# Kernel optimization log

Hardware: AMD Instinct MI355X
Metric: run time of the kernel (lower is better)

## Reference

```python
import jax, jax.numpy as jnp
import numpy as np

DIM = 2048
N_HEADS = 32
N_KV_HEADS = 8
HEAD_DIM = DIM // N_HEADS
N_REP = N_HEADS // N_KV_HEADS
BSZ, SEQ = 2, 2048


def setup_inputs() -> dict:
    key = jax.random.key(0)
    ks = jax.random.split(key, 6)
    hidden_states = jax.random.normal(ks[0], (BSZ, SEQ, DIM), jnp.float32)
    # additive causal mask [1,1,S,S]
    causal = jnp.tril(jnp.ones((SEQ, SEQ), jnp.bool_))
    attention_mask = jnp.where(causal, 0.0, -1e9).astype(jnp.float32)[None, None]
    # RoPE tables [S, head_dim]
    inv_freq = 1.0 / (10000.0 ** (np.arange(0, HEAD_DIM, 2, dtype=np.float32) / HEAD_DIM))
    t = np.arange(SEQ, dtype=np.float32)
    freqs = np.outer(t, inv_freq)  # [S, head_dim/2]
    emb = np.concatenate([freqs, freqs], axis=-1)  # [S, head_dim]
    position_cos = jnp.asarray(np.cos(emb), jnp.float32)
    position_sin = jnp.asarray(np.sin(emb), jnp.float32)
    s = 0.02
    Wq = jax.random.normal(ks[1], (DIM, DIM), jnp.float32) * s
    Wk = jax.random.normal(ks[2], (N_KV_HEADS * HEAD_DIM, DIM), jnp.float32) * s
    Wv = jax.random.normal(ks[3], (N_KV_HEADS * HEAD_DIM, DIM), jnp.float32) * s
    Wo = jax.random.normal(ks[4], (DIM, DIM), jnp.float32) * s
    return {"hidden_states": hidden_states, "attention_mask": attention_mask,
            "position_cos": position_cos, "position_sin": position_sin,
            "Wq": Wq, "Wk": Wk, "Wv": Wv, "Wo": Wo}


def _rotate_half(x):
    x1, x2 = jnp.split(x, 2, axis=-1)
    return jnp.concatenate([-x2, x1], axis=-1)


def _apply_rope(x, cos, sin):
    # x: [b, h, s, d]; cos/sin: [s, d] broadcast over (b, h)
    return x * cos + _rotate_half(x) * sin


def reference(hidden_states, attention_mask, position_cos, position_sin, Wq, Wk, Wv, Wo):
    b, s, _ = hidden_states.shape
    q = jnp.einsum('bsd,ed->bse', hidden_states, Wq).reshape(b, s, N_HEADS, HEAD_DIM).transpose(0, 2, 1, 3)
    k = jnp.einsum('bsd,ed->bse', hidden_states, Wk).reshape(b, s, N_KV_HEADS, HEAD_DIM).transpose(0, 2, 1, 3)
    v = jnp.einsum('bsd,ed->bse', hidden_states, Wv).reshape(b, s, N_KV_HEADS, HEAD_DIM).transpose(0, 2, 1, 3)
    q = _apply_rope(q, position_cos, position_sin)
    k = _apply_rope(k, position_cos, position_sin)
    # GQA: group query heads over kv heads instead of physically repeating k/v
    qg = q.reshape(b, N_KV_HEADS, N_REP, s, HEAD_DIM)
    scores = jnp.einsum('bgrqd,bgkd->bgrqk', qg, k) * (1.0 / jnp.sqrt(jnp.float32(HEAD_DIM)))
    scores = scores + attention_mask[:, :, None, :s, :s]
    weights = jax.nn.softmax(scores.astype(jnp.float32), axis=-1).astype(q.dtype)
    attn = jnp.einsum('bgrqk,bgkd->bgrqd', weights, v)
    attn = attn.reshape(b, N_HEADS, s, HEAD_DIM).transpose(0, 2, 1, 3).reshape(b, s, DIM)
    out = jnp.einsum('bsd,ed->bse', attn, Wo)
    return out
```

## Files before the change

### kernel.cpp

```cpp
#include <hip/hip_runtime.h>
#include <math.h>

#define BSZ 2
#define SEQ 2048
#define DIM 2048
#define NH 32
#define NKV 8
#define HD 64
#define KVDIM 512

typedef short short8 __attribute__((ext_vector_type(8)));
typedef short short4v __attribute__((ext_vector_type(4)));
typedef float f32x4 __attribute__((ext_vector_type(4)));

__device__ __forceinline__ short fbf(float x) {
    unsigned u = __float_as_uint(x);
    u = (u + 0x7fffu + ((u >> 16) & 1u)) >> 16;
    return (short)u;
}
__device__ __forceinline__ short pbf(float x) {
    return (short)((__float_as_uint(x) + 0x8000u) >> 16);
}

#define AS1(p) ((const __attribute__((address_space(1))) void*)(p))
#define AS3(p) ((__attribute__((address_space(3))) void*)(p))

__global__ __launch_bounds__(256) void prep(const float* __restrict__ X,
                                            const float* __restrict__ Wq,
                                            const float* __restrict__ Wk,
                                            const float* __restrict__ Wv,
                                            const float* __restrict__ Wo,
                                            short* __restrict__ Xb,
                                            short* __restrict__ Wqkv,
                                            short* __restrict__ Wob) {
    int i = blockIdx.x * 256 + threadIdx.x;
    const float* src; short* dst; int j;
    if (i < 2097152)      { src = X;  dst = Xb;             j = i; }
    else if (i < 3145728) { src = Wq; dst = Wqkv;           j = i - 2097152; }
    else if (i < 3407872) { src = Wk; dst = Wqkv + 4194304; j = i - 3145728; }
    else if (i < 3670016) { src = Wv; dst = Wqkv + 5242880; j = i - 3407872; }
    else                  { src = Wo; dst = Wob;            j = i - 3670016; }
    float4 f = ((const float4*)src)[j];
    short4v s = { fbf(f.x), fbf(f.y), fbf(f.z), fbf(f.w) };
    ((short4v*)dst)[j] = s;
}

__global__ __launch_bounds__(256) void gemm_qkv(const short* __restrict__ A,
                                                const short* __restrict__ W,
                                                const float* __restrict__ cosT,
                                                const float* __restrict__ sinT,
                                                short* __restrict__ Qo,
                                                short* __restrict__ Ko,
                                                short* __restrict__ Vo) {
    __shared__ short SM[2 * 128 * 64];
    short* As = SM;
    short* Bs = SM + 128 * 64;
    const int K = 2048;
    const int tid = threadIdx.x;
    const int lane = tid & 63, wave = tid >> 6;
    const int l15 = lane & 15, quad = lane >> 4;
    const int m0 = blockIdx.y * 128, n0 = blockIdx.x * 128;
    const int wm = (wave >> 1) * 64, wn = (wave & 1) * 64;
    f32x4 acc[4][4] = {};
    int srow[4], gcol[4];
#pragma unroll
    for (int v = 0; v < 4; ++v) {
        int s = v * 256 + tid;
        srow[v] = s >> 3;
        gcol[v] = ((s & 7) ^ (srow[v] & 7)) * 8;
    }
    for (int kb = 0; kb < K; kb += 64) {
        __syncthreads();
#pragma unroll
        for (int v = 0; v < 4; ++v) {
            int s = v * 256 + tid;
            __builtin_amdgcn_global_load_lds(AS1(A + (size_t)(m0 + srow[v]) * K + kb + gcol[v]),
                                             AS3(&As[s * 8]), 16, 0, 0);
            __builtin_amdgcn_global_load_lds(AS1(W + (size_t)(n0 + srow[v]) * K + kb + gcol[v]),
                                             AS3(&Bs[s * 8]), 16, 0, 0);
        }
        __syncthreads();
#pragma unroll
        for (int kh = 0; kh < 2; ++kh) {
            const int cs = ((kh * 4 + quad) ^ (l15 & 7)) * 8;
            short8 af[4], bf8[4];
#pragma unroll
            for (int i = 0; i < 4; ++i)
                af[i] = *(const short8*)&As[(wm + i * 16 + l15) * 64 + cs];
#pragma unroll
            for (int j = 0; j < 4; ++j)
                bf8[j] = *(const short8*)&Bs[(wn + j * 16 + l15) * 64 + cs];
#pragma unroll
            for (int i = 0; i < 4; ++i)
#pragma unroll
                for (int j = 0; j < 4; ++j)
                    acc[i][j] = __builtin_amdgcn_mfma_f32_16x16x32_bf16(af[i], bf8[j], acc[i][j], 0, 0, 0);
        }
    }
    __syncthreads();
    const int n0r = n0 + wn;
    if (n0r < 2560) {
        short* dst; int heads, hh; float scale;
        if (n0r < 2048) { dst = Qo; heads = NH;  hh = n0r >> 6;          scale = 0.125f * 1.44269504088896f; }
        else            { dst = Ko; heads = NKV; hh = (n0r - 2048) >> 6; scale = 1.0f; }
        short* EB = SM + wave * 4096;
#pragma unroll
        for (int i = 0; i < 4; ++i)
#pragma unroll
            for (int r = 0; r < 4; ++r) {
                int rr = i * 16 + quad * 4 + r;
                int s = (m0 + wm + rr) & (SEQ - 1);
                int msk = ((rr >> 1) & 7) * 8;
#pragma unroll
                for (int jp = 0; jp < 2; ++jp) {
                    int d1 = jp * 16 + l15;
                    float c1 = cosT[s * HD + d1], s1v = sinT[s * HD + d1];
                    float x1 = acc[i][jp][r], x2 = acc[i][jp + 2][r];
                    EB[rr * 64 + (d1 ^ msk)]        = fbf((x1 * c1 - x2 * s1v) * scale);
                    EB[rr * 64 + ((d1 + 32) ^ msk)] = fbf((x2 * c1 + x1 * s1v) * scale);
                }
            }
#pragma unroll
        for (int t = 0; t < 8; ++t) {
            int rr = (lane >> 3) + t * 8;
            int c = lane & 7;
            short8 v8 = *(const short8*)&EB[rr * 64 + c * 8];
            int dchunk = c ^ ((rr >> 1) & 7);
            int mrow = m0 + wm + rr;
            int s = mrow & (SEQ - 1), bb = mrow >> 11;
            *(short8*)&dst[((size_t)(bb * SEQ + s) * heads + hh) * HD + dchunk * 8] = v8;
        }
    } else {
        const int hh = (n0r - 2560) >> 6;
#pragma unroll
        for (int i = 0; i < 4; ++i) {
            int mrow4 = m0 + wm + i * 16 + quad * 4;
            int s_abs = mrow4 & (SEQ - 1);
            int bb = mrow4 >> 11;
            int blk = s_abs >> 6, kk = s_abs & 63;
            int ob = ((kk >> 5) << 3) | (((kk >> 2) & 3) << 1) | ((kk >> 4) & 1);
#pragma unroll
            for (int j = 0; j < 4; ++j) {
                int d = j * 16 + l15;
                short4v pk = { fbf(acc[i][j][0]), fbf(acc[i][j][1]),
                               fbf(acc[i][j][2]), fbf(acc[i][j][3]) };
                *(short4v*)&Vo[(((size_t)(bb * NKV + hh) * HD + d) * SEQ) + blk * 64 + ob * 4] = pk;
            }
        }
    }
}

__global__ __launch_bounds__(256) void gemm_bf16(const short* __restrict__ A,
                                                 const short* __restrict__ W,
                                                 float* __restrict__ C,
                                                 int M, int N, int K) {
    __shared__ short As[128 * 64];
    __shared__ short Bs[128 * 64];
    const int tid = threadIdx.x;
    const int lane = tid & 63, wave = tid >> 6;
    const int l15 = lane & 15, quad = lane >> 4;
    const int m0 = blockIdx.y * 128, n0 = blockIdx.x * 128;
    const int wm = (wave >> 1) * 64, wn = (wave & 1) * 64;
    f32x4 acc[4][4] = {};
    int srow[4], gcol[4];
#pragma unroll
    for (int v = 0; v < 4; ++v) {
        int s = v * 256 + tid;
        srow[v] = s >> 3;
        gcol[v] = ((s & 7) ^ (srow[v] & 7)) * 8;
    }
    for (int kb = 0; kb < K; kb += 64) {
        __syncthreads();
#pragma unroll
        for (int v = 0; v < 4; ++v) {
            int s = v * 256 + tid;
            __builtin_amdgcn_global_load_lds(AS1(A + (size_t)(m0 + srow[v]) * K + kb + gcol[v]),
                                             AS3(&As[s * 8]), 16, 0, 0);
            __builtin_amdgcn_global_load_lds(AS1(W + (size_t)(n0 + srow[v]) * K + kb + gcol[v]),
                                             AS3(&Bs[s * 8]), 16, 0, 0);
        }
        __syncthreads();
#pragma unroll
        for (int kh = 0; kh < 2; ++kh) {
            const int cs = ((kh * 4 + quad) ^ (l15 & 7)) * 8;
            short8 af[4], bf8[4];
#pragma unroll
            for (int i = 0; i < 4; ++i)
                af[i] = *(const short8*)&As[(wm + i * 16 + l15) * 64 + cs];
#pragma unroll
            for (int j = 0; j < 4; ++j)
                bf8[j] = *(const short8*)&Bs[(wn + j * 16 + l15) * 64 + cs];
#pragma unroll
            for (int i = 0; i < 4; ++i)
#pragma unroll
                for (int j = 0; j < 4; ++j)
                    acc[i][j] = __builtin_amdgcn_mfma_f32_16x16x32_bf16(af[i], bf8[j], acc[i][j], 0, 0, 0);
        }
    }
#pragma unroll
    for (int i = 0; i < 4; ++i)
#pragma unroll
        for (int j = 0; j < 4; ++j)
#pragma unroll
            for (int r = 0; r < 4; ++r)
                C[(size_t)(m0 + wm + i * 16 + quad * 4 + r) * N + n0 + wn + j * 16 + l15] = acc[i][j][r];
}

__global__ __launch_bounds__(256, 2) void flash4(const short* __restrict__ Qb,
                                                 const short* __restrict__ Kb,
                                                 const short* __restrict__ VT,
                                                 short* __restrict__ O) {
    __shared__ short Ks[2][128 * 64];
    __shared__ short Vs[2][64 * 128];
    const int bh = blockIdx.x;
    const int qt = (int)gridDim.y - 1 - (int)blockIdx.y;
    const int b = bh >> 5, h = bh & 31, kvh = h >> 2;
    const int tid = threadIdx.x;
    const int wave = tid >> 6, lane = tid & 63;
    const int l15 = lane & 15, quad = lane >> 4;

    short8 qf[2][2];
#pragma unroll
    for (int g = 0; g < 2; ++g) {
        const short* qp = Qb + ((size_t)b * SEQ + qt * 128 + g * 64 + wave * 16 + l15) * DIM + h * HD + quad * 8;
        qf[g][0] = *(const short8*)qp;
        qf[g][1] = *(const short8*)(qp + 32);
    }
    f32x4 o[2][4] = {};
    float m[2] = {-1e30f, -1e30f}, l[2] = {0.f, 0.f};

    const short* Kbase = Kb + (size_t)b * SEQ * KVDIM + kvh * HD;
    const short* Vbase = VT + (size_t)(b * NKV + kvh) * HD * SEQ;

    int krow[4], kcol[4], vrow[4], vcol[4];
#pragma unroll
    for (int v = 0; v < 4; ++v) {
        int s = v * 256 + tid;
        krow[v] = s >> 3;
        kcol[v] = ((s & 7) ^ (krow[v] & 7)) * 8;
        vrow[v] = s >> 4;
        vcol[v] = ((s & 15) ^ (vrow[v] & 7)) * 8;
    }
    auto issue = [&](int kt, int bi) {
#pragma unroll
        for (int v = 0; v < 4; ++v) {
            int s = v * 256 + tid;
            __builtin_amdgcn_global_load_lds(AS1(Kbase + (size_t)(kt * 128 + krow[v]) * KVDIM + kcol[v]),
                                             AS3(&Ks[bi][s * 8]), 16, 0, 0);
            __builtin_amdgcn_global_load_lds(AS1(Vbase + (size_t)vrow[v] * SEQ + kt * 128 + vcol[v]),
                                             AS3(&Vs[bi][s * 8]), 16, 0, 0);
        }
    };
    issue(0, 0);
    const int nkt = qt + 1;
    for (int kt = 0; kt < nkt; ++kt) {
        const int bi = kt & 1;
        __syncthreads();
        if (kt + 1 < nkt) issue(kt + 1, bi ^ 1);

#pragma unroll
        for (int g = 0; g < 2; ++g) {
            const int qmin = qt * 128 + g * 64 + wave * 16;
            f32x4 st[8] = {};
#pragma unroll
            for (int kh = 0; kh < 2; ++kh) {
                const int cs = ((kh * 4 + quad) ^ (l15 & 7)) * 8;
#pragma unroll
                for (int nt = 0; nt < 8; ++nt) {
                    short8 ka = *(const short8*)&Ks[bi][(nt * 16 + l15) * 64 + cs];
                    st[nt] = __builtin_amdgcn_mfma_f32_16x16x32_bf16(ka, qf[g][kh], st[nt], 0, 0, 0);
                }
            }
            if (kt * 128 + 127 > qmin) {
                const int q = qmin + l15;
#pragma unroll
                for (int nt = 0; nt < 8; ++nt)
#pragma unroll
                    for (int r = 0; r < 4; ++r)
                        if (kt * 128 + nt * 16 + quad * 4 + r > q) st[nt][r] = -1e30f;
            }
            float mx = st[0][0];
#pragma unroll
            for (int nt = 0; nt < 8; ++nt)
#pragma unroll
                for (int r = 0; r < 4; ++r) mx = fmaxf(mx, st[nt][r]);
            mx = fmaxf(mx, __shfl_xor(mx, 16));
            mx = fmaxf(mx, __shfl_xor(mx, 32));
            float mn = fmaxf(m[g], mx);
            float al = exp2f(m[g] - mn);
            m[g] = mn;
            float rs = 0.f;
            short8 af[4];
#pragma unroll
            for (int nt = 0; nt < 8; ++nt)
#pragma unroll
                for (int r = 0; r < 4; ++r) {
                    float pv = exp2f(st[nt][r] - mn);
                    rs += pv;
                    af[nt >> 1][(nt & 1) * 4 + r] = pbf(pv);
                }
            rs += __shfl_xor(rs, 16);
            rs += __shfl_xor(rs, 32);
            l[g] = l[g] * al + rs;
            float alr[4];
#pragma unroll
            for (int r = 0; r < 4; ++r) alr[r] = __shfl(al, quad * 4 + r);
#pragma unroll
            for (int dt = 0; dt < 4; ++dt) {
                f32x4 t = o[g][dt];
                t[0] *= alr[0]; t[1] *= alr[1]; t[2] *= alr[2]; t[3] *= alr[3];
#pragma unroll
                for (int kh = 0; kh < 4; ++kh) {
                    const int slot = (kh * 4 + quad) ^ (l15 & 7);
                    short8 vf = *(const short8*)&Vs[bi][(dt * 16 + l15) * 128 + slot * 8];
                    t = __builtin_amdgcn_mfma_f32_16x16x32_bf16(af[kh], vf, t, 0, 0, 0);
                }
                o[g][dt] = t;
            }
        }
    }
#pragma unroll
    for (int g = 0; g < 2; ++g) {
        float lr[4];
#pragma unroll
        for (int r = 0; r < 4; ++r) lr[r] = 1.0f / __shfl(l[g], quad * 4 + r);
        short* Oo = O + ((size_t)b * SEQ + qt * 128 + g * 64 + wave * 16 + quad * 4) * DIM + h * HD + l15;
#pragma unroll
        for (int r = 0; r < 4; ++r)
#pragma unroll
            for (int dt = 0; dt < 4; ++dt)
                Oo[(size_t)r * DIM + dt * 16] = fbf(o[g][dt][r] * lr[r]);
    }
}

extern "C" void kernel_launch(void* const* d_in, const int* in_sizes, int n_in,
                              void* d_out, int out_size, void* d_ws, size_t ws_size,
                              hipStream_t stream) {
    const float* X    = (const float*)d_in[0];
    const float* cosT = (const float*)d_in[2];
    const float* sinT = (const float*)d_in[3];
    const float* Wq   = (const float*)d_in[4];
    const float* Wk   = (const float*)d_in[5];
    const float* Wv   = (const float*)d_in[6];
    const float* Wo   = (const float*)d_in[7];

    char* ws = (char*)d_ws;
    short* Xb    = (short*)(ws);
    short* ATTb  = Xb;
    short* WQKVb = (short*)(ws + 16777216);
    short* Wob   = (short*)(ws + 29360128);
    short* Qbb   = (short*)(ws + 37748736);
    short* Kbb   = (short*)(ws + 54525952);
    short* VTb   = (short*)(ws + 58720256);

    const int M = BSZ * SEQ;
    dim3 blk(256);

    prep<<<dim3(18432), blk, 0, stream>>>(X, Wq, Wk, Wv, Wo, Xb, WQKVb, Wob);
    gemm_qkv<<<dim3(24, M / 128), blk, 0, stream>>>(Xb, WQKVb, cosT, sinT, Qbb, Kbb, VTb);
    flash4<<<dim3(BSZ * NH, SEQ / 128), blk, 0, stream>>>(Qbb, Kbb, VTb, ATTb);
    gemm_bf16<<<dim3(DIM / 128, M / 128), blk, 0, stream>>>(ATTb, Wob, (float*)d_out, M, DIM, DIM);
}
```

Before: 330.9 us.

## Widen flash attention blocks to 256 queries with balanced causal scheduling

The attention kernel now uses 512-thread blocks that each handle 256 query rows, with a remapped grid that pairs long and short causal tiles so that block work is more balanced. Each K/V tile loaded into shared memory is reused by twice as many queries. Waves skip key tiles lying fully above their causal diagonal and only mask the sub-tiles that cross it. The softmax path adds cross-lane reductions via permlane swaps when the compiler provides them, skips the output rescale when the running max is unchanged, uses the hardware exp2 intrinsic, and packs bf16 values with perm instructions. The larger blocks raise register and shared-memory pressure per block, which may reduce occupancy.

```diff
diff --git a/kernel.cpp b/kernel.cpp
--- a/kernel.cpp
+++ b/kernel.cpp
@@ -12,18 +12,55 @@
 typedef short short8 __attribute__((ext_vector_type(8)));
 typedef short short4v __attribute__((ext_vector_type(4)));
 typedef float f32x4 __attribute__((ext_vector_type(4)));
+typedef int i32x4 __attribute__((ext_vector_type(4)));
 
 __device__ __forceinline__ short fbf(float x) {
     unsigned u = __float_as_uint(x);
     u = (u + 0x7fffu + ((u >> 16) & 1u)) >> 16;
     return (short)u;
 }
-__device__ __forceinline__ short pbf(float x) {
-    return (short)((__float_as_uint(x) + 0x8000u) >> 16);
-}
 
 #define AS1(p) ((const __attribute__((address_space(1))) void*)(p))
 #define AS3(p) ((__attribute__((address_space(3))) void*)(p))
+
+#if defined(__has_builtin)
+#if __has_builtin(__builtin_amdgcn_permlane16_swap) && __has_builtin(__builtin_amdgcn_permlane32_swap)
+#define HAVE_PERMLANE 1
+#endif
+#endif
+
+__device__ __forceinline__ float redmax4(float x) {
+#ifdef HAVE_PERMLANE
+    {
+        auto p = __builtin_amdgcn_permlane16_swap(__float_as_uint(x), __float_as_uint(x), false, false);
+        x = fmaxf(__uint_as_float(p[0]), __uint_as_float(p[1]));
+    }
+    {
+        auto p = __builtin_amdgcn_permlane32_swap(__float_as_uint(x), __float_as_uint(x), false, false);
+        x = fmaxf(__uint_as_float(p[0]), __uint_as_float(p[1]));
+    }
+#else
+    x = fmaxf(x, __shfl_xor(x, 16));
+    x = fmaxf(x, __shfl_xor(x, 32));
+#endif
+    return x;
+}
+__device__ __forceinline__ float redsum4(float x) {
+#ifdef HAVE_PERMLANE
+    {
+        auto p = __builtin_amdgcn_permlane16_swap(__float_as_uint(x), __float_as_uint(x), false, false);
+        x = __uint_as_float(p[0]) + __uint_as_float(p[1]);
+    }
+    {
+        auto p = __builtin_amdgcn_permlane32_swap(__float_as_uint(x), __float_as_uint(x), false, false);
+        x = __uint_as_float(p[0]) + __uint_as_float(p[1]);
+    }
+#else
+    x += __shfl_xor(x, 16);
+    x += __shfl_xor(x, 32);
+#endif
+    return x;
+}
 
 __global__ __launch_bounds__(256) void prep(const float* __restrict__ X,
                                             const float* __restrict__ Wq,
@@ -206,14 +243,15 @@
                 C[(size_t)(m0 + wm + i * 16 + quad * 4 + r) * N + n0 + wn + j * 16 + l15] = acc[i][j][r];
 }
 
-__global__ __launch_bounds__(256, 2) void flash4(const short* __restrict__ Qb,
+__global__ __launch_bounds__(512, 4) void flash4(const short* __restrict__ Qb,
                                                  const short* __restrict__ Kb,
                                                  const short* __restrict__ VT,
                                                  short* __restrict__ O) {
     __shared__ short Ks[2][128 * 64];
     __shared__ short Vs[2][64 * 128];
-    const int bh = blockIdx.x;
-    const int qt = (int)gridDim.y - 1 - (int)blockIdx.y;
+    const int d = blockIdx.x + blockIdx.y * 64;
+    const int bh = (d & 255) >> 2;
+    const int qt = (d < 256) ? 7 - (d & 3) : (d & 3);
     const int b = bh >> 5, h = bh & 31, kvh = h >> 2;
     const int tid = threadIdx.x;
     const int wave = tid >> 6, lane = tid & 63;
@@ -222,7 +260,7 @@
     short8 qf[2][2];
 #pragma unroll
     for (int g = 0; g < 2; ++g) {
-        const short* qp = Qb + ((size_t)b * SEQ + qt * 128 + g * 64 + wave * 16 + l15) * DIM + h * HD + quad * 8;
+        const short* qp = Qb + ((size_t)b * SEQ + qt * 256 + g * 128 + wave * 16 + l15) * DIM + h * HD + quad * 8;
         qf[g][0] = *(const short8*)qp;
         qf[g][1] = *(const short8*)(qp + 32);
     }
@@ -232,10 +270,10 @@
     const short* Kbase = Kb + (size_t)b * SEQ * KVDIM + kvh * HD;
     const short* Vbase = VT + (size_t)(b * NKV + kvh) * HD * SEQ;
 
-    int krow[4], kcol[4], vrow[4], vcol[4];
-#pragma unroll
-    for (int v = 0; v < 4; ++v) {
-        int s = v * 256 + tid;
+    int krow[2], kcol[2], vrow[2], vcol[2];
+#pragma unroll
+    for (int v = 0; v < 2; ++v) {
+        int s = v * 512 + tid;
         krow[v] = s >> 3;
         kcol[v] = ((s & 7) ^ (krow[v] & 7)) * 8;
         vrow[v] = s >> 4;
@@ -243,8 +281,8 @@
     }
     auto issue = [&](int kt, int bi) {
 #pragma unroll
-        for (int v = 0; v < 4; ++v) {
-            int s = v * 256 + tid;
+        for (int v = 0; v < 2; ++v) {
+            int s = v * 512 + tid;
             __builtin_amdgcn_global_load_lds(AS1(Kbase + (size_t)(kt * 128 + krow[v]) * KVDIM + kcol[v]),
                                              AS3(&Ks[bi][s * 8]), 16, 0, 0);
             __builtin_amdgcn_global_load_lds(AS1(Vbase + (size_t)vrow[v] * SEQ + kt * 128 + vcol[v]),
@@ -252,7 +290,7 @@
         }
     };
     issue(0, 0);
-    const int nkt = qt + 1;
+    const int nkt = 2 * qt + 2;
     for (int kt = 0; kt < nkt; ++kt) {
         const int bi = kt & 1;
         __syncthreads();
@@ -260,7 +298,8 @@
 
 #pragma unroll
         for (int g = 0; g < 2; ++g) {
-            const int qmin = qt * 128 + g * 64 + wave * 16;
+            const int qmin = qt * 256 + g * 128 + wave * 16;
+            if (kt * 128 > qmin + 15) continue;
             f32x4 st[8] = {};
 #pragma unroll
             for (int kh = 0; kh < 2; ++kh) {
@@ -275,45 +314,64 @@
                 const int q = qmin + l15;
 #pragma unroll
                 for (int nt = 0; nt < 8; ++nt)
-#pragma unroll
-                    for (int r = 0; r < 4; ++r)
-                        if (kt * 128 + nt * 16 + quad * 4 + r > q) st[nt][r] = -1e30f;
-            }
-            float mx = st[0][0];
+                    if (kt * 128 + nt * 16 + 15 > qmin) {
+#pragma unroll
+                        for (int r = 0; r < 4; ++r)
+                            if (kt * 128 + nt * 16 + quad * 4 + r > q) st[nt][r] = -1e30f;
+                    }
+            }
+            float mnt[8];
 #pragma unroll
             for (int nt = 0; nt < 8; ++nt)
-#pragma unroll
-                for (int r = 0; r < 4; ++r) mx = fmaxf(mx, st[nt][r]);
-            mx = fmaxf(mx, __shfl_xor(mx, 16));
-            mx = fmaxf(mx, __shfl_xor(mx, 32));
-            float mn = fmaxf(m[g], mx);
-            float al = exp2f(m[g] - mn);
-            m[g] = mn;
-            float rs = 0.f;
-            short8 af[4];
-#pragma unroll
-            for (int nt = 0; nt < 8; ++nt)
-#pragma unroll
-                for (int r = 0; r < 4; ++r) {
-                    float pv = exp2f(st[nt][r] - mn);
-                    rs += pv;
-                    af[nt >> 1][(nt & 1) * 4 + r] = pbf(pv);
+                mnt[nt] = fmaxf(fmaxf(fmaxf(st[nt][0], st[nt][1]), st[nt][2]), st[nt][3]);
+            float ma = fmaxf(fmaxf(mnt[0], mnt[1]), mnt[2]);
+            float mb = fmaxf(fmaxf(mnt[3], mnt[4]), mnt[5]);
+            float mc = fmaxf(fmaxf(mnt[6], mnt[7]), ma);
+            float mx = redmax4(fmaxf(mb, mc));
+
+            const bool noskip = !__all(mx <= m[g]);
+            float mn = m[g];
+            float al = 1.0f;
+            float alr[4];
+            if (noskip) {
+                mn = fmaxf(m[g], mx);
+                al = __builtin_amdgcn_exp2f(m[g] - mn);
+                m[g] = mn;
+#pragma unroll
+                for (int r = 0; r < 4; ++r) alr[r] = __shfl(al, quad * 4 + r);
+            }
+            i32x4 aw[4];
+            f32x4 rs4 = {};
+#pragma unroll
+            for (int nt = 0; nt < 8; ++nt) {
+                f32x4 pv;
+#pragma unroll
+                for (int r = 0; r < 4; ++r) pv[r] = __builtin_amdgcn_exp2f(st[nt][r] - mn);
+                rs4 += pv;
+                unsigned u0 = __float_as_uint(pv[0]) + 0x8000u;
+                unsigned u1 = __float_as_uint(pv[1]) + 0x8000u;
+                unsigned u2 = __float_as_uint(pv[2]) + 0x8000u;
+                unsigned u3 = __float_as_uint(pv[3]) + 0x8000u;
+                aw[nt >> 1][(nt & 1) * 2 + 0] = (int)__builtin_amdgcn_perm(u1, u0, 0x07060302u);
+                aw[nt >> 1][(nt & 1) * 2 + 1] = (int)__builtin_amdgcn_perm(u3, u2, 0x07060302u);
+            }
+            float rs = redsum4((rs4[0] + rs4[1]) + (rs4[2] + rs4[3]));
+            l[g] = l[g] * al + rs;
+            if (noskip) {
+#pragma unroll
+                for (int dt = 0; dt < 4; ++dt) {
+                    o[g][dt][0] *= alr[0]; o[g][dt][1] *= alr[1];
+                    o[g][dt][2] *= alr[2]; o[g][dt][3] *= alr[3];
                 }
-            rs += __shfl_xor(rs, 16);
-            rs += __shfl_xor(rs, 32);
-            l[g] = l[g] * al + rs;
-            float alr[4];
-#pragma unroll
-            for (int r = 0; r < 4; ++r) alr[r] = __shfl(al, quad * 4 + r);
+            }
 #pragma unroll
             for (int dt = 0; dt < 4; ++dt) {
                 f32x4 t = o[g][dt];
-                t[0] *= alr[0]; t[1] *= alr[1]; t[2] *= alr[2]; t[3] *= alr[3];
 #pragma unroll
                 for (int kh = 0; kh < 4; ++kh) {
                     const int slot = (kh * 4 + quad) ^ (l15 & 7);
                     short8 vf = *(const short8*)&Vs[bi][(dt * 16 + l15) * 128 + slot * 8];
-                    t = __builtin_amdgcn_mfma_f32_16x16x32_bf16(af[kh], vf, t, 0, 0, 0);
+                    t = __builtin_amdgcn_mfma_f32_16x16x32_bf16(__builtin_bit_cast(short8, aw[kh]), vf, t, 0, 0, 0);
                 }
                 o[g][dt] = t;
             }
@@ -321,10 +379,11 @@
     }
 #pragma unroll
     for (int g = 0; g < 2; ++g) {
+        float li = 1.0f / l[g];
         float lr[4];
 #pragma unroll
-        for (int r = 0; r < 4; ++r) lr[r] = 1.0f / __shfl(l[g], quad * 4 + r);
-        short* Oo = O + ((size_t)b * SEQ + qt * 128 + g * 64 + wave * 16 + quad * 4) * DIM + h * HD + l15;
+        for (int r = 0; r < 4; ++r) lr[r] = __shfl(li, quad * 4 + r);
+        short* Oo = O + ((size_t)b * SEQ + qt * 256 + g * 128 + wave * 16 + quad * 4) * DIM + h * HD + l15;
 #pragma unroll
         for (int r = 0; r < 4; ++r)
 #pragma unroll
@@ -358,6 +417,6 @@
 
     prep<<<dim3(18432), blk, 0, stream>>>(X, Wq, Wk, Wv, Wo, Xb, WQKVb, Wob);
     gemm_qkv<<<dim3(24, M / 128), blk, 0, stream>>>(Xb, WQKVb, cosT, sinT, Qbb, Kbb, VTb);
-    flash4<<<dim3(BSZ * NH, SEQ / 128), blk, 0, stream>>>(Qbb, Kbb, VTb, ATTb);
+    flash4<<<dim3(64, 8), dim3(512), 0, stream>>>(Qbb, Kbb, VTb, ATTb);
     gemm_bf16<<<dim3(DIM / 128, M / 128), blk, 0, stream>>>(ATTb, Wob, (float*)d_out, M, DIM, DIM);
 }
```

Measured after the change: 320.8 us. 1.03x faster.
